# Kernel optimization log

Hardware: AMD Instinct MI355X
Metric: run time of the kernel (lower is better)

Reference implementation:

```python
import jax, jax.numpy as jnp
import numpy as np

T = 2048   # block_size
V = 1024   # vocab_size
B = 8


def setup_inputs() -> dict:
    key = jax.random.key(0)
    k_idx, k_v = jax.random.split(key)
    idx = jax.random.randint(k_idx, (B, T), 0, V, dtype=jnp.int64 if jax.config.jax_enable_x64 else jnp.int32)
    # nn.Embedding(4,1) init: normal(mean=0, std=0.02) (the constant init is overwritten)
    v_weight = jax.random.normal(k_v, (4, 1), dtype=jnp.float32) * 0.02
    return {"idx": idx, "v_weight": v_weight}


def reference(idx, v_weight):
    # one-hot token 'embedding': [B, T, V]
    e = jax.nn.one_hot(idx, V, dtype=jnp.float32)

    # relative position table: pos[i,j] = i-j, clamped: <0 -> 3 (padding), >2 -> 2
    r = jnp.arange(T)
    d = r[:, None] - r[None, :]
    pidx = jnp.where(d < 0, 3, jnp.minimum(d, 2))            # [T, T] int

    tril = jnp.tril(jnp.ones((T, T), dtype=jnp.float32))     # lower-triangular mask

    # pos_embd = v(pos).squeeze().tril()
    pos_embd = v_weight[pidx, 0] * tril                      # [T, T]

    # layer_one = pos_embd @ e  -> [B, T, V]
    layer_one = jnp.einsum('ts,bsv->btv', pos_embd, e)

    # attention = e @ layer_one^T -> [B, T, T], then tril mask
    attention = jnp.einsum('btv,bsv->bts', e, layer_one)
    masked_attention = attention * tril                      # broadcast over batch

    # output = masked_attention @ e -> [B, T, V]
    logits = jnp.einsum('bts,bsv->btv', masked_attention, e)

    return jax.nn.softmax(logits, axis=-1)
```

## Files before the change

### kernel.cpp

```cpp
#include <hip/hip_runtime.h>

#define TT   2048
#define VV   1024
#define BB   8
#define ROCC 32

#define SEGP_OFF 0x000000
#define OCC_OFF  0x110000

__global__ __launch_bounds__(1024) void k_pre(const int* __restrict__ idx,
                                              float* __restrict__ SEGP,
                                              int* __restrict__ OCC) {
    __shared__ unsigned h[16][VV];
    const int b = blockIdx.x, tid = threadIdx.x;
    #pragma unroll
    for (int gp = 0; gp < 16; ++gp) h[gp][tid] = 0u;
    __syncthreads();

    const int tok0 = idx[b * TT + tid];
    const int tok1 = idx[b * TT + 1024 + tid];
    const int s0 = tid >> 6;
    const unsigned inc = 1u << ((s0 & 1) * 16);
    atomicAdd(&h[s0 >> 1][tok0], inc);
    atomicAdd(&h[8 + (s0 >> 1)][tok1], inc);
    __syncthreads();

    float* __restrict__ dst = SEGP + (size_t)b * 33 * VV + tid;
    unsigned run = 0;
    #pragma unroll
    for (int gp = 0; gp < 16; ++gp) {
        const unsigned w = h[gp][tid];
        const unsigned b0 = run; run += (w & 0xffffu);
        const unsigned b1 = run; run += (w >> 16);
        h[gp][tid] = b0 | (b1 << 16);
        dst[(2 * gp)     * VV] = (float)b0;
        dst[(2 * gp + 1) * VV] = (float)b1;
    }
    dst[32 * VV] = (float)run;
    __syncthreads();

    const int lane = tid & 63;
    const unsigned long long lt = (lane == 0) ? 0ull : ((~0ull) >> (64 - lane));
    #pragma unroll
    for (int half = 0; half < 2; ++half) {
        const int seg = (tid >> 6) + half * 16;
        const int tok = half ? tok1 : tok0;
        unsigned long long mm = ~0ull;
        #pragma unroll
        for (int bit = 0; bit < 10; ++bit) {
            const unsigned long long bl = __ballot((tok >> bit) & 1);
            mm &= ((tok >> bit) & 1) ? bl : ~bl;
        }
        const int cnt = __popcll(mm & lt);
        const int base = (int)((h[seg >> 1][tok] >> ((seg & 1) * 16)) & 0xffffu);
        const int r0 = base + cnt;
        if (r0 < ROCC) OCC[((size_t)b * VV + tok) * ROCC + r0] = seg * 64 + lane;
    }
}

__global__ __launch_bounds__(64) void k_main(const int* __restrict__ idx,
                                             const float* __restrict__ wt,
                                             const float* __restrict__ SEGP,
                                             const int* __restrict__ OCC,
                                             float* __restrict__ out) {
    __shared__ __align__(16) float slab[VV];
    const int lane = threadIdx.x;
    const int bc = blockIdx.x;
    const int b = bc >> 10, c = bc & (VV - 1);

    const float* __restrict__ segp_b = SEGP + (size_t)b * 33 * VV;
    int m = (int)segp_b[32 * VV + c];
    if (m == 0) return;
    if (m > ROCC) m = ROCC;
    const int* __restrict__ occ = OCC + ((size_t)b * VV + c) * ROCC;
    const int* __restrict__ row = idx + b * TT;
    const float w2 = wt[2], dw0 = wt[0] - w2, dw1 = wt[1] - w2;
    const int myocc = (lane < m) ? occ[lane] : 0;

    const float4 z = {0.0f, 0.0f, 0.0f, 0.0f};
    ((float4*)slab)[lane] = z; ((float4*)slab)[lane +  64] = z;
    ((float4*)slab)[lane + 128] = z; ((float4*)slab)[lane + 192] = z;

    const int cq = c >> 6, cl = c & 63;
    float accM[16];
    #pragma unroll
    for (int q = 0; q < 16; ++q) accM[q] = 0.0f;

    float pendv = 0.0f;
    int   pendtok = 0;
    bool  pend = false;

    for (int K = 1; K <= m; ++K) {
        const float Kf = (float)K;
        const int t = __shfl(myocc, K - 1, 64);
        const int p = t - 1;

        float pr[16];
        int tok = 0;
        float sgn = 0.0f;
        const bool have = (p >= 0);
        if (have) {
            const int g = p >> 6, r = p & 63;
            const int gd = (r < 32) ? g : g + 1;
            const float* __restrict__ prow = segp_b + (size_t)gd * VV;
            #pragma unroll
            for (int q = 0; q < 16; ++q) pr[q] = prow[q * 64 + lane];
            tok = row[(g << 6) + lane];
            sgn = (r < 32) ? ((lane <= r) ? 1.0f : 0.0f)
                           : ((lane >  r) ? -1.0f : 0.0f);
        } else {
            #pragma unroll
            for (int q = 0; q < 16; ++q) pr[q] = 0.0f;
        }

        if (pend)                         atomicAdd(&slab[pendtok], pendv);
        if (have && K > 1 && sgn != 0.0f) atomicAdd(&slab[tok], 64.0f * (Kf - 1.0f) * sgn);
        asm volatile("s_waitcnt lgkmcnt(0)" ::: "memory");

        float acc[16];
        #pragma unroll
        for (int q = 0; q < 16; ++q) {
            const float val = slab[q * 64 + lane];
            const float s  = floorf(val * 0.015625f);
            const float bg = __builtin_fmaf(-64.0f, s, val);
            accM[q] += pr[q];
            float a = w2 * (Kf * pr[q] - accM[q] + s) + dw1 * bg;
            if (q == cq) a += (lane == cl) ? (w2 + dw0) * Kf : 0.0f;
            acc[q] = a;
        }
        pend = (have && sgn != 0.0f);
        pendtok = tok;
        pendv = -64.0f * Kf * sgn;
        if (K < m) {
            const int xn = row[t + 1];
            if (lane == 0) atomicAdd(&slab[xn], 1.0f);
        }

        float mx = -1e30f;
        #pragma unroll
        for (int q = 0; q < 16; ++q) mx = fmaxf(mx, acc[q]);
        #pragma unroll
        for (int o = 32; o > 0; o >>= 1) mx = fmaxf(mx, __shfl_xor(mx, o, 64));
        float sm = 0.0f;
        #pragma unroll
        for (int q = 0; q < 16; ++q) { acc[q] = __expf(acc[q] - mx); sm += acc[q]; }
        #pragma unroll
        for (int o = 32; o > 0; o >>= 1) sm += __shfl_xor(sm, o, 64);
        const float inv = 1.0f / sm;

        float* __restrict__ op = out + (((size_t)b * TT + t) << 10);
        #pragma unroll
        for (int q = 0; q < 16; ++q)
            __builtin_nontemporal_store(acc[q] * inv, &op[q * 64 + lane]);
    }
}

extern "C" void kernel_launch(void* const* d_in, const int* in_sizes, int n_in,
                              void* d_out, int out_size, void* d_ws, size_t ws_size,
                              hipStream_t stream) {
    const int*   idx = (const int*)d_in[0];
    const float* w   = (const float*)d_in[1];
    float*       out = (float*)d_out;
    char* ws = (char*)d_ws;
    float* SEGP = (float*)(ws + SEGP_OFF);
    int*   OCC  = (int*)(ws + OCC_OFF);

    k_pre <<<BB,      1024, 0, stream>>>(idx, SEGP, OCC);
    k_main<<<BB * VV, 64,   0, stream>>>(idx, w, SEGP, OCC, out);
}
```

Baseline: 92.13 us.

## Software-pipeline segment prefix loads and peel first occurrence in main kernel

Peels the K=1 iteration, which needs no shared-slab work, and skips zeroing the slab when a token occurs only once. Inside the loop, the segment-prefix row, token row and next-token loads for iteration K+1 are issued before the current iteration's LDS atomics and softmax, so global-load latency overlaps compute. This adds registers (a second 16-float buffer) and somewhat more complex control flow, which could lower occupancy.

Result: no change. 91.99 us (-0.1%).

```diff
diff --git a/kernel.cpp b/kernel.cpp
--- a/kernel.cpp
+++ b/kernel.cpp
@@ -76,30 +76,21 @@
     const int* __restrict__ row = idx + b * TT;
     const float w2 = wt[2], dw0 = wt[0] - w2, dw1 = wt[1] - w2;
     const int myocc = (lane < m) ? occ[lane] : 0;
-
-    const float4 z = {0.0f, 0.0f, 0.0f, 0.0f};
-    ((float4*)slab)[lane] = z; ((float4*)slab)[lane +  64] = z;
-    ((float4*)slab)[lane + 128] = z; ((float4*)slab)[lane + 192] = z;
-
     const int cq = c >> 6, cl = c & 63;
-    float accM[16];
-    #pragma unroll
-    for (int q = 0; q < 16; ++q) accM[q] = 0.0f;
-
-    float pendv = 0.0f;
-    int   pendtok = 0;
-    bool  pend = false;
-
-    for (int K = 1; K <= m; ++K) {
-        const float Kf = (float)K;
-        const int t = __shfl(myocc, K - 1, 64);
-        const int p = t - 1;
-
-        float pr[16];
-        int tok = 0;
-        float sgn = 0.0f;
-        const bool have = (p >= 0);
-        if (have) {
+
+    if (m > 1) {
+        const float4 z = {0.0f, 0.0f, 0.0f, 0.0f};
+        ((float4*)slab)[lane] = z; ((float4*)slab)[lane +  64] = z;
+        ((float4*)slab)[lane + 128] = z; ((float4*)slab)[lane + 192] = z;
+    }
+
+    float pr[16], prN[16], accM[16];
+
+    int tcur = __shfl(myocc, 0, 64);
+    int tok = 0; float sgn = 0.0f;
+    {
+        const int p = tcur - 1;
+        if (p >= 0) {
             const int g = p >> 6, r = p & 63;
             const int gd = (r < 32) ? g : g + 1;
             const float* __restrict__ prow = segp_b + (size_t)gd * VV;
@@ -112,46 +103,103 @@
             #pragma unroll
             for (int q = 0; q < 16; ++q) pr[q] = 0.0f;
         }
-
-        if (pend)                         atomicAdd(&slab[pendtok], pendv);
-        if (have && K > 1 && sgn != 0.0f) atomicAdd(&slab[tok], 64.0f * (Kf - 1.0f) * sgn);
+    }
+    int tN = 0, tokN = 0, xn = 0; float sgnN = 0.0f;
+    if (m > 1) {
+        tN = __shfl(myocc, 1, 64);
+        const int p = tN - 1;
+        const int g = p >> 6, r = p & 63;
+        const int gd = (r < 32) ? g : g + 1;
+        const float* __restrict__ prow = segp_b + (size_t)gd * VV;
+        #pragma unroll
+        for (int q = 0; q < 16; ++q) prN[q] = prow[q * 64 + lane];
+        tokN = row[(g << 6) + lane];
+        sgnN = (r < 32) ? ((lane <= r) ? 1.0f : 0.0f)
+                        : ((lane >  r) ? -1.0f : 0.0f);
+        xn = row[tcur + 1];
+    }
+    {
+        float mx = -1e30f;
+        #pragma unroll
+        for (int q = 0; q < 16; ++q) {
+            accM[q] = pr[q];
+            float a = 0.0f;
+            if (q == cq) a += (lane == cl) ? (w2 + dw0) : 0.0f;
+            pr[q] = a; mx = fmaxf(mx, a);
+        }
+        #pragma unroll
+        for (int o = 32; o > 0; o >>= 1) mx = fmaxf(mx, __shfl_xor(mx, o, 64));
+        float sm = 0.0f;
+        #pragma unroll
+        for (int q = 0; q < 16; ++q) { const float e = __expf(pr[q] - mx); pr[q] = e; sm += e; }
+        #pragma unroll
+        for (int o = 32; o > 0; o >>= 1) sm += __shfl_xor(sm, o, 64);
+        const float inv = 1.0f / sm;
+        float* __restrict__ op = out + (((size_t)b * TT + tcur) << 10);
+        #pragma unroll
+        for (int q = 0; q < 16; ++q)
+            __builtin_nontemporal_store(pr[q] * inv, &op[q * 64 + lane]);
+    }
+    if (m == 1) return;
+
+    int pendtok = tok; float pendsgn = sgn, pendv = -64.0f * sgn;
+    tcur = tN; tok = tokN; sgn = sgnN;
+    #pragma unroll
+    for (int q = 0; q < 16; ++q) pr[q] = prN[q];
+
+    float Kf = 2.0f;
+    for (int K = 2; K <= m; ++K, Kf += 1.0f) {
+        int xncur = 0;
+        const bool haveN = (K < m);
+        if (haveN) {
+            tN = __shfl(myocc, K, 64);
+            const int p = tN - 1;
+            const int g = p >> 6, r = p & 63;
+            const int gd = (r < 32) ? g : g + 1;
+            const float* __restrict__ prow = segp_b + (size_t)gd * VV;
+            #pragma unroll
+            for (int q = 0; q < 16; ++q) prN[q] = prow[q * 64 + lane];
+            tokN = row[(g << 6) + lane];
+            sgnN = (r < 32) ? ((lane <= r) ? 1.0f : 0.0f)
+                            : ((lane >  r) ? -1.0f : 0.0f);
+            xncur = row[tcur + 1];
+        }
+        if (pendsgn != 0.0f) atomicAdd(&slab[pendtok], pendv);
+        if (sgn != 0.0f)     atomicAdd(&slab[tok], 64.0f * (Kf - 1.0f) * sgn);
+        if (lane == 0)       atomicAdd(&slab[xn], 1.0f);
         asm volatile("s_waitcnt lgkmcnt(0)" ::: "memory");
-
-        float acc[16];
+        float mx = -1e30f;
         #pragma unroll
         for (int q = 0; q < 16; ++q) {
             const float val = slab[q * 64 + lane];
             const float s  = floorf(val * 0.015625f);
             const float bg = __builtin_fmaf(-64.0f, s, val);
             accM[q] += pr[q];
-            float a = w2 * (Kf * pr[q] - accM[q] + s) + dw1 * bg;
+            const float tmp = __builtin_fmaf(Kf, pr[q], s) - accM[q];
+            float a = __builtin_fmaf(w2, tmp, dw1 * bg);
             if (q == cq) a += (lane == cl) ? (w2 + dw0) * Kf : 0.0f;
-            acc[q] = a;
-        }
-        pend = (have && sgn != 0.0f);
-        pendtok = tok;
-        pendv = -64.0f * Kf * sgn;
-        if (K < m) {
-            const int xn = row[t + 1];
-            if (lane == 0) atomicAdd(&slab[xn], 1.0f);
-        }
-
-        float mx = -1e30f;
-        #pragma unroll
-        for (int q = 0; q < 16; ++q) mx = fmaxf(mx, acc[q]);
+            pr[q] = a; mx = fmaxf(mx, a);
+        }
         #pragma unroll
         for (int o = 32; o > 0; o >>= 1) mx = fmaxf(mx, __shfl_xor(mx, o, 64));
         float sm = 0.0f;
         #pragma unroll
-        for (int q = 0; q < 16; ++q) { acc[q] = __expf(acc[q] - mx); sm += acc[q]; }
+        for (int q = 0; q < 16; ++q) { const float e = __expf(pr[q] - mx); pr[q] = e; sm += e; }
         #pragma unroll
         for (int o = 32; o > 0; o >>= 1) sm += __shfl_xor(sm, o, 64);
         const float inv = 1.0f / sm;
-
-        float* __restrict__ op = out + (((size_t)b * TT + t) << 10);
-        #pragma unroll
-        for (int q = 0; q < 16; ++q)
-            __builtin_nontemporal_store(acc[q] * inv, &op[q * 64 + lane]);
+        {
+            float* __restrict__ op = out + (((size_t)b * TT + tcur) << 10);
+            #pragma unroll
+            for (int q = 0; q < 16; ++q)
+                __builtin_nontemporal_store(pr[q] * inv, &op[q * 64 + lane]);
+        }
+        pendtok = tok; pendsgn = sgn; pendv = -64.0f * Kf * sgn;
+        tok = tokN; sgn = sgnN; xn = xncur; tcur = tN;
+        if (haveN) {
+            #pragma unroll
+            for (int q = 0; q < 16; ++q) pr[q] = prN[q];
+        }
     }
 }
 
```
